# Kernel optimization log

Measured on AMD Instinct MI355X. Metric: run time of the kernel, lower is better.

The kernel has to match this reference:

```python
import jax, jax.numpy as jnp
import numpy as np

N = 100000
E = 1600000
IN, HID, OUT = 512, 256, 32
K = 3
LAMBDA_AMP = 0.5


def setup_inputs() -> dict:
    key = jax.random.key(0)
    ks = jax.random.split(key, 6)
    x = jax.random.normal(ks[0], (N, IN), dtype=jnp.float32)
    edge_index = jax.random.randint(ks[1], (2, E), 0, N, dtype=jnp.int64)
    # MLP params (PyTorch Linear default init: U(-1/sqrt(fan_in), 1/sqrt(fan_in)))
    s1 = 1.0 / np.sqrt(IN)
    W1 = jax.random.uniform(ks[2], (IN, HID), jnp.float32, -s1, s1)
    b1 = jax.random.uniform(ks[3], (HID,), jnp.float32, -s1, s1)
    s2 = 1.0 / np.sqrt(HID)
    W2 = jax.random.uniform(ks[4], (HID, OUT), jnp.float32, -s2, s2)
    b2 = jax.random.uniform(ks[5], (OUT,), jnp.float32, -s2, s2)
    return {"x": x, "W1": W1, "b1": b1, "W2": W2, "b2": b2, "edge_index": edge_index}


def _gcn_norm(edge_index, n_nodes, dtype):
    # add self loops, symmetric normalization D^-1/2 (A+I) D^-1/2
    loop = jnp.arange(n_nodes, dtype=edge_index.dtype)
    row = jnp.concatenate([edge_index[0], loop])
    col = jnp.concatenate([edge_index[1], loop])
    w = jnp.ones(row.shape[0], dtype=dtype)
    deg = jax.ops.segment_sum(w, col, num_segments=n_nodes)
    dis = jnp.where(deg > 0, jax.lax.rsqrt(deg), 0.0)
    norm = dis[row] * w * dis[col]
    return row, col, norm


def _proximal_l21(x, lam):
    # row-wise soft-thresholding of L2 norms
    rn = jnp.sqrt(jnp.sum(x * x, axis=1))  # [N]
    safe = jnp.where(rn > 0, rn, 1.0)
    score = jnp.where(rn > 0, jnp.maximum(rn - lam, 0.0) / safe, 0.0)
    return score[:, None] * x


def reference(x, W1, b1, W2, b2, edge_index):
    # MLP (dropout inactive at inference)
    h = jax.nn.relu(x @ W1 + b1)
    h = h @ W2 + b2  # [N, OUT]

    row, col, norm = _gcn_norm(edge_index, N, h.dtype)

    lam = LAMBDA_AMP
    gamma = 1.0 / (2.0 * (1.0 - lam))
    hh = h
    xk = h
    for _ in range(K):
        # A_hat @ xk via gather-scale-scatter
        ax = jax.ops.segment_sum(norm[:, None] * xk[row], col, num_segments=N)
        lx = xk - ax  # L @ xk
        y = xk - gamma * 2.0 * (1.0 - lam) * lx
        xk = hh + _proximal_l21(y - hh, lam * gamma)
    return xk
```

## Files before the change

kernel.cpp:

```cpp
#include <hip/hip_runtime.h>
#include <cstdint>

#define NN 100000
#define EE 1600000
#define IN_F 512
#define HID_F 256
#define OUT_F 32
#define GSL 256
#define SLICE_W 12500
#define CAP 64

typedef float f32x4 __attribute__((ext_vector_type(4)));
typedef int   i32x4 __attribute__((ext_vector_type(4)));
typedef short s16x8 __attribute__((ext_vector_type(8)));
typedef uint32_t u32x4 __attribute__((ext_vector_type(4)));
typedef unsigned short u16;

static __device__ __forceinline__ u16 f2bf(float f) {
  uint32_t u = __builtin_bit_cast(uint32_t, f);
  u += 0x7FFFu + ((u >> 16) & 1u);
  return (u16)(u >> 16);
}

static __device__ __forceinline__ float bf2f(u16 v) {
  uint32_t u = ((uint32_t)v) << 16;
  return __builtin_bit_cast(float, u);
}

static __device__ __forceinline__ uint32_t pk_bf16(float a, float b) {
  uint32_t r;
  asm("v_cvt_pk_bf16_f32 %0, %1, %2" : "=v"(r) : "v"(a), "v"(b));
  return r;
}

__global__ __launch_bounds__(256) void k_prep(const float* __restrict__ w1,
                                              u16* __restrict__ w1f,
                                              const float* __restrict__ w2,
                                              u16* __restrict__ w2f,
                                              int* __restrict__ cur) {
  int b = blockIdx.x;
  int tid = threadIdx.x;
  if (b < 512) {
    int g = b * 256 + tid;
    int j    = g & 7;
    int lane = (g >> 3) & 63;
    int fnG  = (g >> 9) & 15;
    int kk   = g >> 13;
    int k = kk * 32 + (lane >> 4) * 8 + j;
    int n = fnG * 16 + (lane & 15);
    w1f[g] = f2bf(w1[k * HID_F + n]);
  } else if (b < 544) {
    int g = (b - 512) * 256 + tid;
    int j    = g & 7;
    int lane = (g >> 3) & 63;
    int ff   = g >> 9;
    int k = (ff >> 1) * 32 + (lane >> 4) * 8 + j;
    int n = (ff & 1) * 16 + (lane & 15);
    w2f[g] = f2bf(w2[k * OUT_F + n]);
  } else {
    int i = (b - 544) * 256 + tid;
    if (i < NN) cur[i] = 0;
  }
}

__global__ __launch_bounds__(256) void k_fillC(const int* __restrict__ row,
                                               const int* __restrict__ col,
                                               int* __restrict__ cur,
                                               int* __restrict__ csr) {
  const int slice = blockIdx.x & 7;
  const int g = blockIdx.x >> 3;
  const unsigned lo = (unsigned)slice * SLICE_W, hi = lo + SLICE_W;
  const i32x4* c4 = (const i32x4*)col;
  const i32x4* r4 = (const i32x4*)row;
  for (int i = g * 256 + threadIdx.x; i < EE / 4; i += GSL * 256) {
    i32x4 c = c4[i];
    i32x4 r = r4[i];
    #pragma unroll
    for (int k = 0; k < 4; ++k) {
      unsigned cc = (unsigned)c[k];
      if (cc >= lo && cc < hi) {
        int p = atomicAdd(&cur[cc], 1);
        if (p < CAP) csr[(int)cc * CAP + p] = r[k];
      }
    }
  }
}

__global__ __launch_bounds__(512) void k_mlp(
    const float* __restrict__ x, const float* __restrict__ b1,
    const float* __restrict__ b2, const u16* __restrict__ w1f,
    const u16* __restrict__ w2f, const int* __restrict__ cnt,
    float* __restrict__ hout, u16* __restrict__ xs0) {
  __shared__ char smem[131072];
  char* aL  = smem;
  char* h1L = smem;

  const int tid  = threadIdx.x;
  const int lane = tid & 63;
  const int wid  = tid >> 6;
  const int wm   = wid >> 2;
  const int wn   = wid & 3;
  const int l16  = lane & 15;
  const int lq   = lane >> 4;
  const int row0 = blockIdx.x * 128;

  const f32x4 zf = {0.f, 0.f, 0.f, 0.f};

  #pragma unroll
  for (int rr = 0; rr < 16; ++rr) {
    int row  = wid * 16 + rr;
    int grow = row0 + row;
    f32x4 a0 = zf, a1 = zf;
    if (grow < NN) {
      const float* xp = x + (size_t)grow * IN_F + lane * 8;
      a0 = *(const f32x4*)xp;
      a1 = *(const f32x4*)(xp + 4);
    }
    u32x4 pk;
    pk.x = pk_bf16(a0.x, a0.y);
    pk.y = pk_bf16(a0.z, a0.w);
    pk.z = pk_bf16(a1.x, a1.y);
    pk.w = pk_bf16(a1.z, a1.w);
    int slot = lane ^ (row & 7);
    *(u32x4*)(aL + row * 1024 + slot * 16) = pk;
  }
  __syncthreads();

  f32x4 acc[4][4];
  #pragma unroll
  for (int i = 0; i < 4; ++i)
    #pragma unroll
    for (int j = 0; j < 4; ++j) acc[i][j] = zf;

  const int abase = wm * 64;

  s16x8 bf[4], bfn[4];
  #pragma unroll
  for (int fn = 0; fn < 4; ++fn)
    bf[fn] = *(const s16x8*)(w1f + ((size_t)(0 * 16 + wn * 4 + fn) * 64 + lane) * 8);

  #pragma unroll
  for (int kk = 0; kk < 16; ++kk) {
    if (kk < 15) {
      #pragma unroll
      for (int fn = 0; fn < 4; ++fn)
        bfn[fn] = *(const s16x8*)(w1f + ((size_t)((kk + 1) * 16 + wn * 4 + fn) * 64 + lane) * 8);
    }
    s16x8 af[4];
    #pragma unroll
    for (int fm = 0; fm < 4; ++fm) {
      int row  = abase + fm * 16 + l16;
      int slot = (kk * 4 + lq) ^ (row & 7);
      af[fm] = *(const s16x8*)(aL + row * 1024 + slot * 16);
    }
    #pragma unroll
    for (int fm = 0; fm < 4; ++fm)
      #pragma unroll
      for (int fn = 0; fn < 4; ++fn)
        acc[fm][fn] = __builtin_amdgcn_mfma_f32_16x16x32_bf16(
            af[fm], bf[fn], acc[fm][fn], 0, 0, 0);
    #pragma unroll
    for (int fn = 0; fn < 4; ++fn) bf[fn] = bfn[fn];
  }

  float b1v[4];
  #pragma unroll
  for (int fn = 0; fn < 4; ++fn) b1v[fn] = b1[wn * 64 + fn * 16 + l16];

  __syncthreads();
  #pragma unroll
  for (int fm = 0; fm < 4; ++fm) {
    #pragma unroll
    for (int fn = 0; fn < 4; ++fn) {
      int col = wn * 64 + fn * 16 + l16;
      #pragma unroll
      for (int r = 0; r < 4; ++r) {
        int row = wm * 64 + fm * 16 + lq * 4 + r;
        float v = acc[fm][fn][r] + b1v[fn];
        v = fmaxf(v, 0.f);
        *(u16*)(h1L + row * 512 + ((col * 2) ^ ((row & 7) << 4))) = f2bf(v);
      }
    }
  }
  __syncthreads();

  f32x4 acc2[2];
  acc2[0] = zf; acc2[1] = zf;
  const int arow = wid * 16 + l16;
  #pragma unroll
  for (int ks = 0; ks < 8; ++ks) {
    int kb = ks * 64 + lq * 16;
    s16x8 af = *(const s16x8*)(h1L + arow * 512 + (kb ^ ((arow & 7) << 4)));
    #pragma unroll
    for (int fn = 0; fn < 2; ++fn) {
      s16x8 bfr = *(const s16x8*)(w2f + ((size_t)((ks * 2 + fn) * 64) + lane) * 8);
      acc2[fn] = __builtin_amdgcn_mfma_f32_16x16x32_bf16(af, bfr, acc2[fn], 0, 0, 0);
    }
  }
  #pragma unroll
  for (int r = 0; r < 4; ++r) {
    int row = row0 + wid * 16 + lq * 4 + r;
    if (row >= NN) continue;
    float dr = rsqrtf((float)cnt[row] + 1.0f);
    #pragma unroll
    for (int fn = 0; fn < 2; ++fn) {
      int col = fn * 16 + l16;
      float v = acc2[fn][r] + b2[col];
      hout[(size_t)row * 32 + col] = v;
      xs0[(size_t)row * 32 + col] = f2bf(dr * v);
    }
  }
}

template <int LAST>
__global__ __launch_bounds__(256) void k_prop(
    const u16* __restrict__ xs, const float* __restrict__ hh,
    u16* __restrict__ xs_out, float* __restrict__ fout,
    const int* __restrict__ cnt, const int* __restrict__ csr) {
  int w = blockIdx.x * 4 + (threadIdx.x >> 6);
  if (w >= NN) return;
  const int lane = threadIdx.x & 63;
  const int q = lane & 3;
  const int s = lane >> 2;
  const int n = cnt[w];
  const int* __restrict__ crow = csr + (size_t)w * CAP;
  float acc[8] = {0.f, 0.f, 0.f, 0.f, 0.f, 0.f, 0.f, 0.f};
  for (int j = s; j < n; j += 16) {
    int src = crow[j];
    s16x8 v = *(const s16x8*)(xs + (size_t)src * 32 + q * 8);
    #pragma unroll
    for (int k = 0; k < 8; ++k) acc[k] += bf2f((u16)v[k]);
  }
  if (s == 0) {
    s16x8 v = *(const s16x8*)(xs + (size_t)w * 32 + q * 8);
    #pragma unroll
    for (int k = 0; k < 8; ++k) acc[k] += bf2f((u16)v[k]);
  }
  #pragma unroll
  for (int m = 4; m <= 32; m <<= 1) {
    #pragma unroll
    for (int k = 0; k < 8; ++k) acc[k] += __shfl_xor(acc[k], m, 64);
  }
  const float di = rsqrtf((float)n + 1.0f);
  const f32x4 h0 = *(const f32x4*)(hh + (size_t)w * 32 + q * 8);
  const f32x4 h1 = *(const f32x4*)(hh + (size_t)w * 32 + q * 8 + 4);
  float hv[8] = {h0.x, h0.y, h0.z, h0.w, h1.x, h1.y, h1.z, h1.w};
  float d[8];
  float rn2 = 0.f;
  #pragma unroll
  for (int k = 0; k < 8; ++k) {
    d[k] = di * acc[k] - hv[k];
    rn2 += d[k] * d[k];
  }
  rn2 += __shfl_xor(rn2, 1, 64);
  rn2 += __shfl_xor(rn2, 2, 64);
  float rn = sqrtf(rn2);
  float sc = (rn > 0.f) ? fmaxf(rn - 0.5f, 0.f) / rn : 0.f;
  if (s == 0) {
    if (LAST) {
      f32x4 o0, o1;
      o0.x = hv[0] + sc * d[0]; o0.y = hv[1] + sc * d[1];
      o0.z = hv[2] + sc * d[2]; o0.w = hv[3] + sc * d[3];
      o1.x = hv[4] + sc * d[4]; o1.y = hv[5] + sc * d[5];
      o1.z = hv[6] + sc * d[6]; o1.w = hv[7] + sc * d[7];
      *(f32x4*)(fout + (size_t)w * 32 + q * 8) = o0;
      *(f32x4*)(fout + (size_t)w * 32 + q * 8 + 4) = o1;
    } else {
      s16x8 o;
      #pragma unroll
      for (int k = 0; k < 8; ++k) o[k] = (short)f2bf(di * (hv[k] + sc * d[k]));
      *(s16x8*)(xs_out + (size_t)w * 32 + q * 8) = o;
    }
  }
}

extern "C" void kernel_launch(void* const* d_in, const int* in_sizes, int n_in,
                              void* d_out, int out_size, void* d_ws, size_t ws_size,
                              hipStream_t stream) {
  const float* x  = (const float*)d_in[0];
  const float* W1 = (const float*)d_in[1];
  const float* b1 = (const float*)d_in[2];
  const float* W2 = (const float*)d_in[3];
  const float* b2 = (const float*)d_in[4];
  const int*   ei = (const int*)d_in[5];

  char* ws = (char*)d_ws;
  float* h    = (float*)(ws);
  u16*   xs0  = (u16*)  (ws + 12800000);
  u16*   xs1  = (u16*)  (ws + 19200000);
  int*   csr  = (int*)  (ws + 25600000);
  int*   cur  = (int*)  (ws + 51200000);
  u16*   w1f  = (u16*)  (ws + 51600000);
  u16*   w2f  = (u16*)  (ws + 51862144);

  k_prep<<<935, 256, 0, stream>>>(W1, w1f, W2, w2f, cur);
  k_fillC<<<8 * GSL, 256, 0, stream>>>(ei, ei + EE, cur, csr);
  k_mlp<<<(NN + 127) / 128, 512, 0, stream>>>(x, b1, b2, w1f, w2f, cur, h, xs0);

  float* out = (float*)d_out;
  k_prop<0><<<(NN + 3) / 4, 256, 0, stream>>>(xs0, h, xs1, nullptr, cur, csr);
  k_prop<0><<<(NN + 3) / 4, 256, 0, stream>>>(xs1, h, xs0, nullptr, cur, csr);
  k_prop<1><<<(NN + 3) / 4, 256, 0, stream>>>(xs0, h, nullptr, out,  cur, csr);
}
```

Before: 296.4 us.

## Shrink MLP tile to 64 rows and stream x through LDS in K-slices

```diff
diff --git a/kernel.cpp b/kernel.cpp
--- a/kernel.cpp
+++ b/kernel.cpp
@@ -86,81 +86,68 @@
   }
 }
 
-__global__ __launch_bounds__(512) void k_mlp(
+__global__ __launch_bounds__(256, 4) void k_mlp(
     const float* __restrict__ x, const float* __restrict__ b1,
     const float* __restrict__ b2, const u16* __restrict__ w1f,
     const u16* __restrict__ w2f, const int* __restrict__ cnt,
     float* __restrict__ hout, u16* __restrict__ xs0) {
-  __shared__ char smem[131072];
+  __shared__ char smem[32768];
   char* aL  = smem;
   char* h1L = smem;
 
   const int tid  = threadIdx.x;
   const int lane = tid & 63;
   const int wid  = tid >> 6;
-  const int wm   = wid >> 2;
-  const int wn   = wid & 3;
+  const int wn   = wid;
   const int l16  = lane & 15;
   const int lq   = lane >> 4;
-  const int row0 = blockIdx.x * 128;
+  const int row0 = blockIdx.x * 64;
 
   const f32x4 zf = {0.f, 0.f, 0.f, 0.f};
-
-  #pragma unroll
-  for (int rr = 0; rr < 16; ++rr) {
-    int row  = wid * 16 + rr;
-    int grow = row0 + row;
-    f32x4 a0 = zf, a1 = zf;
-    if (grow < NN) {
-      const float* xp = x + (size_t)grow * IN_F + lane * 8;
-      a0 = *(const f32x4*)xp;
-      a1 = *(const f32x4*)(xp + 4);
-    }
-    u32x4 pk;
-    pk.x = pk_bf16(a0.x, a0.y);
-    pk.y = pk_bf16(a0.z, a0.w);
-    pk.z = pk_bf16(a1.x, a1.y);
-    pk.w = pk_bf16(a1.z, a1.w);
-    int slot = lane ^ (row & 7);
-    *(u32x4*)(aL + row * 1024 + slot * 16) = pk;
-  }
-  __syncthreads();
-
   f32x4 acc[4][4];
   #pragma unroll
   for (int i = 0; i < 4; ++i)
     #pragma unroll
     for (int j = 0; j < 4; ++j) acc[i][j] = zf;
 
-  const int abase = wm * 64;
-
-  s16x8 bf[4], bfn[4];
-  #pragma unroll
-  for (int fn = 0; fn < 4; ++fn)
-    bf[fn] = *(const s16x8*)(w1f + ((size_t)(0 * 16 + wn * 4 + fn) * 64 + lane) * 8);
-
-  #pragma unroll
-  for (int kk = 0; kk < 16; ++kk) {
-    if (kk < 15) {
+  for (int kt = 0; kt < IN_F / 64; ++kt) {
+    __syncthreads();
+    #pragma unroll
+    for (int p = 0; p < 4; ++p) {
+      int v   = p * 256 + tid;
+      int row = v >> 4;
+      int f4  = v & 15;
+      int grow = row0 + row;
+      f32x4 xv = zf;
+      if (grow < NN)
+        xv = *(const f32x4*)(x + (size_t)grow * IN_F + kt * 64 + f4 * 4);
+      uint32_t lo = pk_bf16(xv.x, xv.y);
+      uint32_t hi = pk_bf16(xv.z, xv.w);
+      uint64_t wv = (uint64_t)lo | ((uint64_t)hi << 32);
+      int kb = (f4 * 8) ^ ((row & 7) << 4);
+      *(uint64_t*)(aL + row * 128 + kb) = wv;
+    }
+    __syncthreads();
+    #pragma unroll
+    for (int ks = 0; ks < 2; ++ks) {
+      const int kk = kt * 2 + ks;
+      s16x8 af[4], bf[4];
       #pragma unroll
       for (int fn = 0; fn < 4; ++fn)
-        bfn[fn] = *(const s16x8*)(w1f + ((size_t)((kk + 1) * 16 + wn * 4 + fn) * 64 + lane) * 8);
-    }
-    s16x8 af[4];
-    #pragma unroll
-    for (int fm = 0; fm < 4; ++fm) {
-      int row  = abase + fm * 16 + l16;
-      int slot = (kk * 4 + lq) ^ (row & 7);
-      af[fm] = *(const s16x8*)(aL + row * 1024 + slot * 16);
-    }
-    #pragma unroll
-    for (int fm = 0; fm < 4; ++fm)
-      #pragma unroll
-      for (int fn = 0; fn < 4; ++fn)
-        acc[fm][fn] = __builtin_amdgcn_mfma_f32_16x16x32_bf16(
-            af[fm], bf[fn], acc[fm][fn], 0, 0, 0);
-    #pragma unroll
-    for (int fn = 0; fn < 4; ++fn) bf[fn] = bfn[fn];
+        bf[fn] = *(const s16x8*)(w1f + ((size_t)(kk * 16 + wn * 4 + fn) * 64 + lane) * 8);
+      #pragma unroll
+      for (int fm = 0; fm < 4; ++fm) {
+        int row = fm * 16 + l16;
+        int kb  = (ks * 64 + lq * 16) ^ ((row & 7) << 4);
+        af[fm] = *(const s16x8*)(aL + row * 128 + kb);
+      }
+      #pragma unroll
+      for (int fm = 0; fm < 4; ++fm)
+        #pragma unroll
+        for (int fn = 0; fn < 4; ++fn)
+          acc[fm][fn] = __builtin_amdgcn_mfma_f32_16x16x32_bf16(
+              af[fm], bf[fn], acc[fm][fn], 0, 0, 0);
+    }
   }
 
   float b1v[4];
@@ -175,7 +162,7 @@
       int col = wn * 64 + fn * 16 + l16;
       #pragma unroll
       for (int r = 0; r < 4; ++r) {
-        int row = wm * 64 + fm * 16 + lq * 4 + r;
+        int row = fm * 16 + lq * 4 + r;
         float v = acc[fm][fn][r] + b1v[fn];
         v = fmaxf(v, 0.f);
         *(u16*)(h1L + row * 512 + ((col * 2) ^ ((row & 7) << 4))) = f2bf(v);
@@ -295,7 +282,7 @@
 
   k_prep<<<935, 256, 0, stream>>>(W1, w1f, W2, w2f, cur);
   k_fillC<<<8 * GSL, 256, 0, stream>>>(ei, ei + EE, cur, csr);
-  k_mlp<<<(NN + 127) / 128, 512, 0, stream>>>(x, b1, b2, w1f, w2f, cur, h, xs0);
+  k_mlp<<<(NN + 63) / 64, 256, 0, stream>>>(x, b1, b2, w1f, w2f, cur, h, xs0);
 
   float* out = (float*)d_out;
   k_prop<0><<<(NN + 3) / 4, 256, 0, stream>>>(xs0, h, xs1, nullptr, cur, csr);
```

After: 276.7 us. 6.7% less time.
